# Kernel optimization log

Measured on AMD Instinct MI355X. Metric: run time of the kernel, lower is better.

The kernel has to match this reference:

```python
import jax, jax.numpy as jnp
import numpy as np

BATCH, IN_SIZE, CH, DIM, MODES, LAYERS, PROJ, OUT = 16, 1, 128, 128, 32, 4, 128, 1


def setup_inputs() -> dict:
    key = jax.random.key(0)
    ks = jax.random.split(key, 12)
    scale = 1.0 / (CH * CH)
    inp = {
        "z": jax.random.normal(ks[0], (BATCH, IN_SIZE, DIM, DIM), dtype=jnp.float32),
        # Lifting: pointwise linear input_size -> channels
        "lift_w": jax.random.normal(ks[1], (CH, IN_SIZE), dtype=jnp.float32) / np.sqrt(IN_SIZE),
        "lift_b": jnp.zeros((CH,), dtype=jnp.float32),
        # Spectral conv weights per layer, two mode corners, complex stored as real/imag
        "wr1": scale * jax.random.normal(ks[2], (LAYERS, CH, CH, MODES, MODES), dtype=jnp.float32),
        "wi1": scale * jax.random.normal(ks[3], (LAYERS, CH, CH, MODES, MODES), dtype=jnp.float32),
        "wr2": scale * jax.random.normal(ks[4], (LAYERS, CH, CH, MODES, MODES), dtype=jnp.float32),
        "wi2": scale * jax.random.normal(ks[5], (LAYERS, CH, CH, MODES, MODES), dtype=jnp.float32),
        # Projection: channels -> projection_size -> output_size (pointwise MLP)
        "pw1": jax.random.normal(ks[6], (PROJ, CH), dtype=jnp.float32) / np.sqrt(CH),
        "pb1": jnp.zeros((PROJ,), dtype=jnp.float32),
        "pw2": jax.random.normal(ks[7], (OUT, PROJ), dtype=jnp.float32) / np.sqrt(PROJ),
        "pb2": jnp.zeros((OUT,), dtype=jnp.float32),
    }
    return inp


def _spectral_conv(v, w1, w2, modes, size):
    # v: [b, c, X, Y] real; rfft2 over last two dims (norm='backward')
    vf = jnp.fft.rfft2(v, norm="backward")  # [b, c, X, Y//2+1] complex
    of = jnp.zeros_like(vf)
    # low-frequency corner
    of = of.at[:, :, :modes, :modes].set(
        jnp.einsum("bixy,ioxy->boxy", vf[:, :, :modes, :modes], w1))
    # high (negative) frequency corner along first spatial axis
    of = of.at[:, :, -modes:, :modes].set(
        jnp.einsum("bixy,ioxy->boxy", vf[:, :, -modes:, :modes], w2))
    return jnp.fft.irfft2(of, s=(size, size), norm="backward")


def reference(z, lift_w, lift_b, wr1, wi1, wr2, wi2, pw1, pb1, pw2, pb2):
    n_layers = wr1.shape[0]
    modes = wr1.shape[-1]
    size = z.shape[-1]
    # Lifting: [b, in, x, y] -> [b, ch, x, y]
    v = jnp.einsum("bixy,ci->bcxy", z, lift_w) + lift_b[None, :, None, None]
    out = v
    for l in range(n_layers):
        w1 = wr1[l] + 1j * wi1[l]
        w2 = wr2[l] + 1j * wi2[l]
        out = _spectral_conv(out, w1, w2, modes, size)
    # Projection MLP (pointwise over grid)
    h = jnp.einsum("bcxy,pc->bpxy", out, pw1) + pb1[None, :, None, None]
    h = jax.nn.gelu(h)
    out = jnp.einsum("bpxy,op->boxy", h, pw2) + pb2[None, :, None, None]
    return out
```

## Files before the change

kernel.cpp:

```cpp
#include <hip/hip_runtime.h>
#include <math.h>

#define B 16
#define CH 128
#define DIM 128
#define MODES 32
#define NLAYERS 4
#define PROJ 128
#define U 64
#define KY 32
#define NMODE (U*KY)
#define N2 (DIM*DIM)
#define PG 32
#define PPG (PROJ/PG)

__device__ __forceinline__ void async16(const void* g, void* l) {
  __builtin_amdgcn_global_load_lds((const __attribute__((address_space(1))) unsigned int*)g,
                                   (__attribute__((address_space(3))) unsigned int*)l, 16, 0, 0);
}

__global__ __launch_bounds__(256) void k_zf1(const float* __restrict__ z,
                                             float2* __restrict__ t1) {
  __shared__ float zrow[16][DIM];
  __shared__ float2 tw[DIM];
  int bid = blockIdx.x;
  int b = bid >> 3, xt = bid & 7;
  int x0 = xt * 16;
  int t = threadIdx.x;
  if (t < 128) {
    float ang = (float)(2.0 * M_PI) * (float)t / 128.0f;
    tw[t] = make_float2(cosf(ang), sinf(ang));
  }
  for (int e = t; e < 16 * DIM / 4; e += 256)
    ((float4*)&zrow[0][0])[e] = ((const float4*)&z[b * N2 + x0 * DIM])[e];
  __syncthreads();
  #pragma unroll
  for (int j = 0; j < 2; ++j) {
    int it = t + j * 256;
    int x_l = it >> 5, ky = it & 31;
    float tr = 0.f, ti = 0.f;
    for (int y = 0; y < DIM; ++y) {
      float v = zrow[x_l][y];
      float2 w = tw[(ky * y) & 127];
      tr += v * w.x;
      ti -= v * w.y;
    }
    t1[((size_t)b * DIM + x0 + x_l) * KY + ky] = make_float2(tr, ti);
  }
}

__global__ __launch_bounds__(256) void k_zf2(const float2* __restrict__ t1,
                                             float* __restrict__ zfr, float* __restrict__ zfi) {
  __shared__ float2 t1s[DIM][KY];
  __shared__ float2 tw[DIM];
  int bid = blockIdx.x;
  int b = bid >> 1, uh = bid & 1;
  int t = threadIdx.x;
  if (t < 128) {
    float ang = (float)(2.0 * M_PI) * (float)t / 128.0f;
    tw[t] = make_float2(cosf(ang), sinf(ang));
  }
  for (int e = t; e < DIM * KY / 2; e += 256)
    ((float4*)&t1s[0][0])[e] = ((const float4*)&t1[(size_t)b * DIM * KY])[e];
  __syncthreads();
  #pragma unroll
  for (int j = 0; j < 4; ++j) {
    int m = t + j * 256;
    int u_l = m >> 5, ky = m & 31;
    int u = uh * 32 + u_l;
    int kx = (u < 32) ? u : (u + 64);
    float ar = 0.f, ai = 0.f;
    for (int x = 0; x < DIM; ++x) {
      float2 v = t1s[x][ky];
      float2 w = tw[(kx * x) & 127];
      ar += v.x * w.x + v.y * w.y;
      ai += v.y * w.x - v.x * w.y;
    }
    zfr[b * NMODE + u * KY + ky] = ar;
    zfi[b * NMODE + u * KY + ky] = ai;
  }
}

__global__ __launch_bounds__(256) void k_lift(const float* __restrict__ zfr, const float* __restrict__ zfi,
                                              const float* __restrict__ lw, const float* __restrict__ lb,
                                              float2* __restrict__ vcout) {
  int idx = blockIdx.x * 256 + threadIdx.x;
  if (idx >= B * CH * NMODE) return;
  int m = idx & (NMODE - 1);
  int c = (idx >> 11) & 127;
  int b = idx >> 18;
  float w = lw[c];
  float re = w * zfr[b * NMODE + m];
  float im = w * zfi[b * NMODE + m];
  if (m == 0) re += 16384.f * lb[c];
  vcout[idx] = make_float2(re, im);
}

__global__ __launch_bounds__(256) void k_spec(const float2* __restrict__ vc,
                                              const float* __restrict__ wr1, const float* __restrict__ wi1,
                                              const float* __restrict__ wr2, const float* __restrict__ wi2,
                                              float2* __restrict__ oc) {
  __shared__ float  lW[2][4][8][32];
  __shared__ float2 lV[2][2][8][32];
  int bid = blockIdx.x;
  int u = ((bid & 7) << 3) | ((bid >> 3) & 7);
  int rest = bid >> 6;
  int o0 = (rest & 15) * 8;
  int b0 = (rest >> 4) * 8;
  int kxw = u & 31;
  const float* wr = (u >= 32) ? wr2 : wr1;
  const float* wi = (u >= 32) ? wi2 : wi1;
  int t = threadIdx.x;
  int ky = t & 31, q = t >> 5;
  int oh = q >> 2, bq = q & 3;
  int wv = t >> 6, lane = t & 63;
  float accR[4][2] = {}, accI[4][2] = {};

  #define STAGE(bf, i0)                                                              \
    {                                                                                \
      _Pragma("unroll")                                                              \
      for (int n = 0; n < 2; ++n) {                                                  \
        int nu = wv * 2 + n;                                                         \
        if (nu < 4) {                                                                \
          int ri = nu >> 1, il = nu & 1;                                             \
          int o_l = lane >> 3, ky4 = (lane & 7) * 4;                                 \
          const float* src = (ri ? wi : wr) +                                        \
            (((size_t)((i0) + il) * CH + o0 + o_l) * MODES + kxw) * MODES + ky4;     \
          async16(src, (char*)&lW[bf][0][0][0] + (size_t)nu * 1024 + lane * 16);     \
        } else {                                                                     \
          int nv = nu - 4;                                                           \
          int il = nv >> 1, h = nv & 1;                                              \
          int b_l = h * 4 + (lane >> 4), ky2 = (lane & 15) * 2;                      \
          const float2* src = vc + ((size_t)(b0 + b_l) * CH + (i0) + il) * NMODE +   \
                              u * KY + ky2;                                          \
          async16(src, (char*)&lV[bf][0][0][0] + (size_t)nv * 1024 + lane * 16);     \
        }                                                                            \
      }                                                                              \
    }

  #define COMPUTE(bf)                                                                \
    {                                                                                \
      _Pragma("unroll")                                                              \
      for (int il = 0; il < 2; ++il) {                                               \
        float wrv[4], wiv[4];                                                        \
        _Pragma("unroll")                                                            \
        for (int j = 0; j < 4; ++j) {                                                \
          wrv[j] = lW[bf][il][oh * 4 + j][ky];                                       \
          wiv[j] = lW[bf][2 + il][oh * 4 + j][ky];                                   \
        }                                                                            \
        _Pragma("unroll")                                                            \
        for (int bb = 0; bb < 2; ++bb) {                                             \
          float2 v = lV[bf][il][bq * 2 + bb][ky];                                    \
          _Pragma("unroll")                                                          \
          for (int j = 0; j < 4; ++j) {                                              \
            accR[j][bb] += wrv[j] * v.x - wiv[j] * v.y;                              \
            accI[j][bb] += wrv[j] * v.y + wiv[j] * v.x;                              \
          }                                                                          \
        }                                                                            \
      }                                                                              \
    }

  STAGE(0, 0);
  for (int k = 0; k < 64; ++k) {
    int cur = k & 1;
    __syncthreads();
    if (k + 1 < 64) STAGE(cur ^ 1, (k + 1) * 2);
    COMPUTE(cur);
  }
  #undef STAGE
  #undef COMPUTE
  #pragma unroll
  for (int j = 0; j < 4; ++j)
    #pragma unroll
    for (int bb = 0; bb < 2; ++bb) {
      int o = o0 + oh * 4 + j, b = b0 + bq * 2 + bb;
      oc[(((size_t)b * CH + o) * U + u) * KY + ky] = make_float2(accR[j][bb], accI[j][bb]);
    }
}

__global__ __launch_bounds__(256) void k_proj0(float2* __restrict__ vc) {
  int idx = blockIdx.x * 256 + threadIdx.x;
  if (idx >= B * CH * 33) return;
  int pi = idx % 33;
  int bc = idx / 33;
  float2* base = vc + (size_t)bc * NMODE;
  if (pi == 0) {
    base[0].y = 0.f;
  } else if (pi == 32) {
    base[32 * KY].x *= 0.5f;
    base[32 * KY].y *= 0.5f;
  } else {
    int ua = pi, ub = 64 - pi;
    float2 a = base[ua * KY], b2 = base[ub * KY];
    base[ua * KY] = make_float2(0.5f * (a.x + b2.x), 0.5f * (a.y - b2.y));
    base[ub * KY] = make_float2(0.5f * (b2.x + a.x), 0.5f * (b2.y - a.y));
  }
}

__global__ __launch_bounds__(256) void k_pw1(const float2* __restrict__ xc,
                                             const float* __restrict__ pw1,
                                             float2* __restrict__ hc) {
  __shared__ float wT[CH][CH + 1];
  int bid = blockIdx.x;
  int b = ((bid & 7) << 1) | ((bid >> 8) & 1);
  int jt = (bid >> 3) & 31;
  int t = threadIdx.x;
  for (int e = t; e < CH * CH; e += 256) {
    int p = e >> 7, c = e & 127;
    wT[c][p] = pw1[e];
  }
  __syncthreads();
  int tx = t & 15, ty = t >> 4;
  int j0 = jt * 64 + tx * 4;
  float accR[4][8] = {}, accI[4][8] = {};
  for (int c = 0; c < CH; ++c) {
    const float4* x4 = (const float4*)&xc[((size_t)b * CH + c) * NMODE + j0];
    float4 v0 = x4[0], v1 = x4[1];
    float xrv[4] = {v0.x, v0.z, v1.x, v1.z};
    float xiv[4] = {v0.y, v0.w, v1.y, v1.w};
    float w[8];
    #pragma unroll
    for (int pp = 0; pp < 8; ++pp) w[pp] = wT[c][ty * 8 + pp];
    #pragma unroll
    for (int jj = 0; jj < 4; ++jj)
      #pragma unroll
      for (int pp = 0; pp < 8; ++pp) {
        accR[jj][pp] += w[pp] * xrv[jj];
        accI[jj][pp] += w[pp] * xiv[jj];
      }
  }
  #pragma unroll
  for (int pp = 0; pp < 8; ++pp) {
    int p = ty * 8 + pp;
    float4* o4 = (float4*)&hc[((size_t)b * CH + p) * NMODE + j0];
    o4[0] = make_float4(accR[0][pp], accI[0][pp], accR[1][pp], accI[1][pp]);
    o4[1] = make_float4(accR[2][pp], accI[2][pp], accR[3][pp], accI[3][pp]);
  }
}

__global__ __launch_bounds__(256) void k_idft_partial(const float2* __restrict__ hc,
                                                      const float* __restrict__ pb1,
                                                      const float* __restrict__ pw2,
                                                      float* __restrict__ partial) {
  __shared__ float2 tw[DIM];
  __shared__ float2 hfs[2][NMODE];
  __shared__ float2 sbuf[16][KY];
  __shared__ float4 sE[8][32];
  int bid = blockIdx.x;
  int b = (bid & 7) | (((bid >> 3) & 1) << 3);
  int pg = (bid >> 4) & 31, xs = bid >> 9;
  int x0 = xs * 8;
  int t = threadIdx.x;
  int wv = t >> 6, lane = t & 63;
  if (t < 128) {
    float ang = (float)(2.0 * M_PI) * (float)t / 128.0f;
    tw[t] = make_float2(cosf(ang), sinf(ang));
  }

  #define STAGE_H(bf, pp_)                                                           \
    {                                                                                \
      const char* srcb = (const char*)(hc + ((size_t)b * CH + pg * PPG + (pp_)) * NMODE); \
      _Pragma("unroll")                                                              \
      for (int n = 0; n < 4; ++n) {                                                  \
        int nu = wv * 4 + n;                                                         \
        async16(srcb + (size_t)nu * 1024 + lane * 16,                                \
                (char*)&hfs[bf][0] + (size_t)nu * 1024 + lane * 16);                 \
      }                                                                              \
    }

  STAGE_H(0, 0);
  __syncthreads();
  {
    int xq = t >> 5, j = t & 31;
    int x = x0 + xq;
    int kxE = (j < 16) ? (2 * j) : (2 * j + 64);
    float2 wE = tw[(kxE * x) & 127];
    float2 wO = tw[((kxE + 1) * x) & 127];
    sE[xq][j] = make_float4(wE.x, wE.y, wO.x, wO.y);
  }
  int y = t & 63, xh = t >> 6;
  float Cr[KY], Sr[KY];
  #pragma unroll
  for (int ky = 0; ky < KY; ++ky) {
    float2 w = tw[(ky * y) & 127];
    float wk = (ky == 0) ? 1.f : 2.f;
    Cr[ky] = wk * w.x;
    Sr[ky] = -wk * w.y;
  }
  __syncthreads();
  int xqA = t >> 5, kyA = t & 31;
  float res[8] = {0.f, 0.f, 0.f, 0.f, 0.f, 0.f, 0.f, 0.f};
  for (int pp = 0; pp < PPG; ++pp) {
    int p = pg * PPG + pp;
    int cur = pp & 1;
    if (pp) __syncthreads();
    if (pp + 1 < PPG) STAGE_H(cur ^ 1, pp + 1);
    {
      float per = 0.f, pei = 0.f, por = 0.f, poi = 0.f;
      #pragma unroll
      for (int j = 0; j < 32; ++j) {
        float4 E = sE[xqA][j];
        float2 h0 = hfs[cur][(2 * j) * KY + kyA];
        float2 h1 = hfs[cur][(2 * j + 1) * KY + kyA];
        per += h0.x * E.x - h0.y * E.y;
        pei += h0.x * E.y + h0.y * E.x;
        por += h1.x * E.z - h1.y * E.w;
        poi += h1.x * E.w + h1.y * E.z;
      }
      sbuf[xqA][kyA]     = make_float2(per + por, pei + poi);
      sbuf[xqA + 8][kyA] = make_float2(per - por, pei - poi);
    }
    __syncthreads();
    float pb = pb1[p], pw = pw2[p];
    #pragma unroll
    for (int sl = 0; sl < 4; ++sl) {
      int s_i = xh + sl * 4;
      float ae = 0.f, ao = 0.f;
      #pragma unroll
      for (int ky = 0; ky < KY; ky += 2) {
        float4 v = *(const float4*)&sbuf[s_i][ky];
        ae += v.x * Cr[ky] + v.y * Sr[ky];
        ao += v.z * Cr[ky + 1] + v.w * Sr[ky + 1];
      }
      float hlo = (ae + ao) * (1.f / 16384.f) + pb;
      float hhi = (ae - ao) * (1.f / 16384.f) + pb;
      float zlo = 1.5957691216057308f * (hlo + 0.044715f * hlo * hlo * hlo);
      float zhi = 1.5957691216057308f * (hhi + 0.044715f * hhi * hhi * hhi);
      res[sl * 2]     += pw * hlo * __builtin_amdgcn_rcpf(1.f + __expf(-zlo));
      res[sl * 2 + 1] += pw * hhi * __builtin_amdgcn_rcpf(1.f + __expf(-zhi));
    }
  }
  #undef STAGE_H
  size_t pbase = ((size_t)pg * B + b) * N2;
  #pragma unroll
  for (int sl = 0; sl < 4; ++sl) {
    int s_i = xh + sl * 4;
    int x = x0 + (s_i & 7) + ((s_i >> 3) << 6);
    partial[pbase + x * DIM + y]      = res[sl * 2];
    partial[pbase + x * DIM + y + 64] = res[sl * 2 + 1];
  }
}

__global__ __launch_bounds__(256) void k_reduce(const float* __restrict__ partial,
                                                const float* __restrict__ pb2,
                                                float* __restrict__ outp) {
  int idx = blockIdx.x * 256 + threadIdx.x;
  if (idx >= B * N2) return;
  float s = pb2[0];
  #pragma unroll
  for (int pg = 0; pg < PG; ++pg) s += partial[(size_t)pg * B * N2 + idx];
  outp[idx] = s;
}

extern "C" void kernel_launch(void* const* d_in, const int* in_sizes, int n_in,
                              void* d_out, int out_size, void* d_ws, size_t ws_size,
                              hipStream_t stream) {
  const float* z   = (const float*)d_in[0];
  const float* lw  = (const float*)d_in[1];
  const float* lb  = (const float*)d_in[2];
  const float* wr1 = (const float*)d_in[3];
  const float* wi1 = (const float*)d_in[4];
  const float* wr2 = (const float*)d_in[5];
  const float* wi2 = (const float*)d_in[6];
  const float* pw1 = (const float*)d_in[7];
  const float* pb1 = (const float*)d_in[8];
  const float* pw2 = (const float*)d_in[9];
  const float* pb2 = (const float*)d_in[10];
  float* out = (float*)d_out;
  float* ws = (float*)d_ws;

  float* zfr = ws;
  float* zfi = zfr + 32768;
  float2* Ac = (float2*)(ws + 65536);
  float2* Bc = Ac + (size_t)B * CH * NMODE;
  float2* t1 = Bc;

  k_zf1<<<B * 8, 256, 0, stream>>>(z, t1);
  k_zf2<<<B * 2, 256, 0, stream>>>(t1, zfr, zfi);
  k_lift<<<(B * CH * NMODE) / 256, 256, 0, stream>>>(zfr, zfi, lw, lb, Ac);

  const size_t WSTRIDE = (size_t)CH * CH * MODES * MODES;
  float2 *ir = Ac, *oc = Bc;
  for (int l = 0; l < NLAYERS; ++l) {
    k_spec<<<2048, 256, 0, stream>>>(ir,
                                     wr1 + l * WSTRIDE, wi1 + l * WSTRIDE,
                                     wr2 + l * WSTRIDE, wi2 + l * WSTRIDE,
                                     oc);
    if (l < NLAYERS - 1)
      k_proj0<<<(B * CH * 33 + 255) / 256, 256, 0, stream>>>(oc);
    float2* tmp = ir; ir = oc; oc = tmp;
  }
  k_pw1<<<512, 256, 0, stream>>>(ir, pw1, oc);
  float* partial = (float*)ir;
  k_idft_partial<<<B * PG * 8, 256, 0, stream>>>(oc, pb1, pw2, partial);
  k_reduce<<<(B * N2) / 256, 256, 0, stream>>>(partial, pb2, out);
}
```

Before: 918.5 us.

## Retile spectral contraction to cover all batches per block and halve the ky span

The k_spec tiling changes from 8 outputs × 8 batches × 32 ky per block to 16 outputs × all 16 batches × 16 ky, so each weight element is loaded from global memory once instead of twice (once per batch half). The per-thread accumulator grows from 4x2 to 4x4 complex values, and the grid shrinks from 2048 to 1024 blocks. This targets the weight traffic, which dominates the spectral layer, at the cost of more registers per thread and fewer, shorter-row global accesses (64-byte ky segments instead of 128-byte).

```diff
diff --git a/kernel.cpp b/kernel.cpp
--- a/kernel.cpp
+++ b/kernel.cpp
@@ -100,21 +100,21 @@
                                               const float* __restrict__ wr1, const float* __restrict__ wi1,
                                               const float* __restrict__ wr2, const float* __restrict__ wi2,
                                               float2* __restrict__ oc) {
-  __shared__ float  lW[2][4][8][32];
-  __shared__ float2 lV[2][2][8][32];
+  __shared__ float  lW[2][2][2][16][16];
+  __shared__ float2 lV[2][2][16][16];
   int bid = blockIdx.x;
   int u = ((bid & 7) << 3) | ((bid >> 3) & 7);
   int rest = bid >> 6;
-  int o0 = (rest & 15) * 8;
-  int b0 = (rest >> 4) * 8;
+  int ot = rest & 7, kyh = rest >> 3;
+  int o0 = ot * 16;
+  int ky0 = kyh * 16;
   int kxw = u & 31;
   const float* wr = (u >= 32) ? wr2 : wr1;
   const float* wi = (u >= 32) ? wi2 : wi1;
   int t = threadIdx.x;
-  int ky = t & 31, q = t >> 5;
-  int oh = q >> 2, bq = q & 3;
+  int ky = t & 15, oh = (t >> 4) & 3, bq = t >> 6;
   int wv = t >> 6, lane = t & 63;
-  float accR[4][2] = {}, accI[4][2] = {};
+  float accR[4][4] = {}, accI[4][4] = {};
 
   #define STAGE(bf, i0)                                                              \
     {                                                                                \
@@ -123,16 +123,17 @@
         int nu = wv * 2 + n;                                                         \
         if (nu < 4) {                                                                \
           int ri = nu >> 1, il = nu & 1;                                             \
-          int o_l = lane >> 3, ky4 = (lane & 7) * 4;                                 \
+          int o_l = lane >> 2, kyq = lane & 3;                                       \
           const float* src = (ri ? wi : wr) +                                        \
-            (((size_t)((i0) + il) * CH + o0 + o_l) * MODES + kxw) * MODES + ky4;     \
-          async16(src, (char*)&lW[bf][0][0][0] + (size_t)nu * 1024 + lane * 16);     \
+            (((size_t)((i0) + il) * CH + o0 + o_l) * MODES + kxw) * MODES +          \
+            ky0 + kyq * 4;                                                           \
+          async16(src, (char*)&lW[bf][0][0][0][0] + (size_t)nu * 1024 + lane * 16);  \
         } else {                                                                     \
           int nv = nu - 4;                                                           \
-          int il = nv >> 1, h = nv & 1;                                              \
-          int b_l = h * 4 + (lane >> 4), ky2 = (lane & 15) * 2;                      \
-          const float2* src = vc + ((size_t)(b0 + b_l) * CH + (i0) + il) * NMODE +   \
-                              u * KY + ky2;                                          \
+          int il = nv >> 1, bhf = nv & 1;                                            \
+          int b_l = bhf * 8 + (lane >> 3), kyd = lane & 7;                           \
+          const float2* src = vc + ((size_t)b_l * CH + (i0) + il) * NMODE +          \
+                              u * KY + ky0 + kyd * 2;                                \
           async16(src, (char*)&lV[bf][0][0][0] + (size_t)nv * 1024 + lane * 16);     \
         }                                                                            \
       }                                                                              \
@@ -145,12 +146,12 @@
         float wrv[4], wiv[4];                                                        \
         _Pragma("unroll")                                                            \
         for (int j = 0; j < 4; ++j) {                                                \
-          wrv[j] = lW[bf][il][oh * 4 + j][ky];                                       \
-          wiv[j] = lW[bf][2 + il][oh * 4 + j][ky];                                   \
+          wrv[j] = lW[bf][0][il][oh * 4 + j][ky];                                    \
+          wiv[j] = lW[bf][1][il][oh * 4 + j][ky];                                    \
         }                                                                            \
         _Pragma("unroll")                                                            \
-        for (int bb = 0; bb < 2; ++bb) {                                             \
-          float2 v = lV[bf][il][bq * 2 + bb][ky];                                    \
+        for (int bb = 0; bb < 4; ++bb) {                                             \
+          float2 v = lV[bf][il][bq * 4 + bb][ky];                                    \
           _Pragma("unroll")                                                          \
           for (int j = 0; j < 4; ++j) {                                              \
             accR[j][bb] += wrv[j] * v.x - wiv[j] * v.y;                              \
@@ -172,9 +173,9 @@
   #pragma unroll
   for (int j = 0; j < 4; ++j)
     #pragma unroll
-    for (int bb = 0; bb < 2; ++bb) {
-      int o = o0 + oh * 4 + j, b = b0 + bq * 2 + bb;
-      oc[(((size_t)b * CH + o) * U + u) * KY + ky] = make_float2(accR[j][bb], accI[j][bb]);
+    for (int bb = 0; bb < 4; ++bb) {
+      int o = o0 + oh * 4 + j, b = bq * 4 + bb;
+      oc[(((size_t)b * CH + o) * U + u) * KY + ky0 + ky] = make_float2(accR[j][bb], accI[j][bb]);
     }
 }
 
@@ -382,7 +383,7 @@
   const size_t WSTRIDE = (size_t)CH * CH * MODES * MODES;
   float2 *ir = Ac, *oc = Bc;
   for (int l = 0; l < NLAYERS; ++l) {
-    k_spec<<<2048, 256, 0, stream>>>(ir,
+    k_spec<<<1024, 256, 0, stream>>>(ir,
                                      wr1 + l * WSTRIDE, wi1 + l * WSTRIDE,
                                      wr2 + l * WSTRIDE, wi2 + l * WSTRIDE,
                                      oc);
```

New measurement: 770.9 us, median of 2. -16.1%, faster.
